# Kernel optimization log

Measured on AMD Instinct MI355X. Metric: run time of the kernel, lower is better.

## Reference

```python
import jax, jax.numpy as jnp
import numpy as np
import math

EPS = 1e-5  # torch LayerNorm default
B, T, H, W, C = 2, 16, 32, 32, 768
NH = 12
HD = C // NH


def layernorm(x, w, b):
    mu = jnp.mean(x, axis=-1, keepdims=True)
    var = jnp.var(x, axis=-1, keepdims=True)
    return (x - mu) * jax.lax.rsqrt(var + EPS) * w + b


def setup_inputs() -> dict:
    key = jax.random.key(0)
    ks = jax.random.split(key, 4)
    s = 1.0 / math.sqrt(C)
    return {
        "x": jax.random.normal(ks[0], (B, T, H, W, C), dtype=jnp.float32),
        "ln1_w": jnp.ones((C,), jnp.float32),
        "ln1_b": jnp.zeros((C,), jnp.float32),
        "Wqkv": jax.random.normal(ks[1], (3 * C, C), jnp.float32) * s,
        "bqkv": jnp.zeros((3 * C,), jnp.float32),
        "ln2_w": jnp.ones((C,), jnp.float32),
        "ln2_b": jnp.zeros((C,), jnp.float32),
        "Wout": jax.random.normal(ks[2], (C, C), jnp.float32) * s,
        "bout": jnp.zeros((C,), jnp.float32),
    }


def reference(x, ln1_w, ln1_b, Wqkv, bqkv, ln2_w, ln2_b, Wout, bout):
    b, t, h, w, c = x.shape
    inp = x
    y = layernorm(x, ln1_w, ln1_b)
    qkv = jnp.einsum('bthwc,fc->bthwf', y, Wqkv) + bqkv          # (B,T,H,W,3C)
    qkv = qkv.reshape(b, t, h, w, NH, 3 * HD)
    q, k, v = jnp.split(qkv, 3, axis=-1)                          # each (B,T,H,W,NH,HD)
    scale = 1.0 / math.sqrt(HD)
    # attention over the time axis, batched over (b,h,w,heads)
    scores = jnp.einsum('bthwnd,bshwnd->bhwnts', q, k) * scale    # (B,H,W,NH,T,T)
    attn = jax.nn.softmax(scores, axis=-1)
    o = jnp.einsum('bhwnts,bshwnd->bthwnd', attn, v)              # (B,T,H,W,NH,HD)
    o = o.reshape(b, t, h, w, c)
    o = layernorm(o, ln2_w, ln2_b)
    o = jnp.einsum('bthwc,fc->bthwf', o, Wout) + bout
    return o + inp
```

## Files before the change

### kernel.cpp

```cpp
#include <hip/hip_runtime.h>

typedef unsigned short u16;
typedef __attribute__((ext_vector_type(8))) short frag8;
typedef __attribute__((ext_vector_type(4))) float f32x4;

static constexpr int C = 768;
static constexpr int F3 = 2304;
static constexpr int MROWS = 32768;
static constexpr float LNEPS = 1e-5f;

__device__ __forceinline__ float bfu2f(u16 u){
  union { unsigned u; float f; } x; x.u = (unsigned)u << 16; return x.f;
}
__device__ __forceinline__ u16 f2bfu(float f){
  union { float f; unsigned u; } x; x.f = f;
  unsigned r = x.u + 0x7fffu + ((x.u >> 16) & 1u);
  return (u16)(r >> 16);
}

__device__ __forceinline__ void gload16(const void* g, void* l){
  __builtin_amdgcn_global_load_lds(
      (const __attribute__((address_space(1))) void*)g,
      (__attribute__((address_space(3))) void*)l, 16, 0, 0);
}

__global__ __launch_bounds__(256) void cvt_bf16(const float* __restrict__ src,
                                                u16* __restrict__ dst, int n){
  int i = blockIdx.x * 256 + threadIdx.x;
  if (i < n) dst[i] = f2bfu(src[i]);
}

__global__ __launch_bounds__(256) void ln1_kernel(const float* __restrict__ x,
    const float* __restrict__ w, const float* __restrict__ b, u16* __restrict__ y){
  const int lane = threadIdx.x & 63, wid = threadIdx.x >> 6;
  const size_t row = (size_t)blockIdx.x * 4 + wid;
  const float4* xr = reinterpret_cast<const float4*>(x + row * C);
  float v[12];
  #pragma unroll
  for (int j = 0; j < 3; j++){
    float4 t = xr[lane + j*64];
    v[j*4+0]=t.x; v[j*4+1]=t.y; v[j*4+2]=t.z; v[j*4+3]=t.w;
  }
  float s = 0.f, ss = 0.f;
  #pragma unroll
  for (int j = 0; j < 12; j++){ s += v[j]; ss += v[j]*v[j]; }
  #pragma unroll
  for (int o = 32; o; o >>= 1){ s += __shfl_xor(s, o, 64); ss += __shfl_xor(ss, o, 64); }
  const float mu = s * (1.f/768.f);
  const float rs = rsqrtf(ss*(1.f/768.f) - mu*mu + LNEPS);
  ushort4* yr = reinterpret_cast<ushort4*>(y + row * C);
  const float4* wv = reinterpret_cast<const float4*>(w);
  const float4* bv = reinterpret_cast<const float4*>(b);
  #pragma unroll
  for (int j = 0; j < 3; j++){
    float4 wj = wv[lane + j*64], bj = bv[lane + j*64];
    ushort4 o4;
    o4.x = f2bfu((v[j*4+0]-mu)*rs*wj.x + bj.x);
    o4.y = f2bfu((v[j*4+1]-mu)*rs*wj.y + bj.y);
    o4.z = f2bfu((v[j*4+2]-mu)*rs*wj.z + bj.z);
    o4.w = f2bfu((v[j*4+3]-mu)*rs*wj.w + bj.w);
    yr[lane + j*64] = o4;
  }
}

template<int MODE>
__global__ __launch_bounds__(256, 2) void gemm_bt(
    const u16* __restrict__ A, const u16* __restrict__ Bw,
    const float* __restrict__ bias, const float* __restrict__ resid,
    void* __restrict__ Cout, int Ndim, int K)
{
  __shared__ __align__(16) char lds[49152];
  const int tid = threadIdx.x;
  const int lane = tid & 63, wn = tid >> 6;
  const int ntn = Ndim >> 8;
  const int cpx = (int)gridDim.x >> 3;
  const int wg = ((int)blockIdx.x & 7) * cpx + ((int)blockIdx.x >> 3);
  const int bm = wg / ntn, bn = wg % ntn;
  const int m0 = bm << 7, n0 = bn << 8;

  const int rp = lane >> 2;
  const int rr = rp ^ ((rp >> 2) & 1);
  const int qq = (lane & 3) ^ (rr & 3);
  const u16* aS = A  + (size_t)(m0 + rr) * K + qq*8;
  const u16* bS = Bw + (size_t)(n0 + rr) * K + qq*8;
  const size_t rgK = 16 * (size_t)K;

  const int fr = lane & 15, kq = lane >> 4;
  const int sig16 = (((fr ^ ((fr >> 2) & 1)) << 2) | (kq ^ (fr & 3))) * 16;

  f32x4 acc[8][4] = {};

  auto stage = [&](int ts){
    char* lb = lds + (ts & 1)*24576;
    const u16* a = aS + ts*32;
    const u16* b = bS + ts*32;
    gload16(a + (size_t)(2*wn    )*rgK, lb + (2*wn    )*1024);
    gload16(a + (size_t)(2*wn + 1)*rgK, lb + (2*wn + 1)*1024);
    #pragma unroll
    for (int i = 0; i < 4; i++)
      gload16(b + (size_t)(4*wn + i)*rgK, lb + 8192 + (4*wn + i)*1024);
  };

  stage(0);

  for (int t = 0; t < 24; ++t){
    int tn = t + 1; if (tn >= 24) tn = 0;
    stage(tn);
    asm volatile("s_waitcnt vmcnt(6)" ::: "memory");
    __builtin_amdgcn_s_barrier();

    const char* base = lds + (t & 1)*24576;
    const char* pb = base + 8192 + (wn*4)*1024 + sig16;
    frag8 af[8], bf[4];
    #pragma unroll
    for (int nf = 0; nf < 4; nf++) bf[nf] = *reinterpret_cast<const frag8*>(pb + nf*1024);
    #pragma unroll
    for (int mf = 0; mf < 8; mf++) af[mf] = *reinterpret_cast<const frag8*>(base + mf*1024 + sig16);
    asm volatile("s_waitcnt lgkmcnt(0)" ::: "memory");
    __builtin_amdgcn_sched_barrier(0);
    __builtin_amdgcn_s_setprio(1);
    #pragma unroll
    for (int mf = 0; mf < 8; mf++)
      #pragma unroll
      for (int nf = 0; nf < 4; nf++)
        acc[mf][nf] = __builtin_amdgcn_mfma_f32_16x16x32_bf16(bf[nf], af[mf], acc[mf][nf], 0, 0, 0);
    __builtin_amdgcn_s_setprio(0);
    __builtin_amdgcn_s_barrier();
  }
  asm volatile("s_waitcnt vmcnt(0)" ::: "memory");

  const int em = fr, en = kq * 4;
  float4 bb[4];
  #pragma unroll
  for (int nf = 0; nf < 4; nf++)
    bb[nf] = *reinterpret_cast<const float4*>(bias + n0 + wn*64 + nf*16 + en);

  #pragma unroll
  for (int mf = 0; mf < 8; mf++){
    const size_t m = (size_t)(m0 + mf*16 + em);
    #pragma unroll
    for (int nf = 0; nf < 4; nf++){
      const int n = n0 + wn*64 + nf*16 + en;
      if (MODE == 0){
        ushort4 o4;
        o4.x = f2bfu(acc[mf][nf][0] + bb[nf].x);
        o4.y = f2bfu(acc[mf][nf][1] + bb[nf].y);
        o4.z = f2bfu(acc[mf][nf][2] + bb[nf].z);
        o4.w = f2bfu(acc[mf][nf][3] + bb[nf].w);
        *reinterpret_cast<ushort4*>((u16*)Cout + m * Ndim + n) = o4;
      } else {
        const float4 rr4 = *reinterpret_cast<const float4*>(resid + m * Ndim + n);
        float4 o4;
        o4.x = acc[mf][nf][0] + bb[nf].x + rr4.x;
        o4.y = acc[mf][nf][1] + bb[nf].y + rr4.y;
        o4.z = acc[mf][nf][2] + bb[nf].z + rr4.z;
        o4.w = acc[mf][nf][3] + bb[nf].w + rr4.w;
        *reinterpret_cast<float4*>((float*)Cout + m * Ndim + n) = o4;
      }
    }
  }
}

__global__ __launch_bounds__(256) void attn_ln2(const u16* __restrict__ qkv,
    const float* __restrict__ w2, const float* __restrict__ b2, u16* __restrict__ y2){
  __shared__ __align__(16) u16 S[16][2312];
  __shared__ float SP[4][16][17];
  const int tid = threadIdx.x;
  const int lane = tid & 63, wid = tid >> 6;
  const int bid = blockIdx.x;
  const int w = bid & 31, h = (bid >> 5) & 31, b = bid >> 10;
  const size_t rbase = (size_t)b*16384 + h*32 + w;

  #pragma unroll
  for (int it = 0; it < 18; it++){
    const int e = tid + it*256;
    const int t = e / 288, c = e % 288;
    const uint4 v = *reinterpret_cast<const uint4*>(qkv + (rbase + (size_t)t*1024)*F3 + c*8);
    *reinterpret_cast<uint4*>(&S[t][c*8]) = v;
  }
  __syncthreads();

  const int g = lane >> 4, sj = lane & 15;
  #pragma unroll
  for (int hh = 0; hh < 3; hh++){
    const int n = wid*3 + hh;
    const int q0 = n*192, k0 = q0 + 64, v0 = q0 + 128;
    float accv[4] = {0.f, 0.f, 0.f, 0.f};
    #pragma unroll
    for (int dc = 0; dc < 8; dc++){
      union { uint4 u; u16 s[8]; } kc;
      kc.u = *reinterpret_cast<const uint4*>(&S[sj][k0 + dc*8]);
      #pragma unroll
      for (int i = 0; i < 4; i++){
        union { uint4 u; u16 s[8]; } qc;
        qc.u = *reinterpret_cast<const uint4*>(&S[g + 4*i][q0 + dc*8]);
        #pragma unroll
        for (int e = 0; e < 8; e++)
          accv[i] += bfu2f(qc.s[e]) * bfu2f(kc.s[e]);
      }
    }
    #pragma unroll
    for (int i = 0; i < 4; i++){
      float sc = accv[i] * 0.125f;
      float mx = sc;
      #pragma unroll
      for (int o = 1; o < 16; o <<= 1) mx = fmaxf(mx, __shfl_xor(mx, o, 16));
      float p = __expf(sc - mx);
      float sm = p;
      #pragma unroll
      for (int o = 1; o < 16; o <<= 1) sm += __shfl_xor(sm, o, 16);
      SP[wid][g + 4*i][sj] = p / sm;
    }
    float ot[16];
    #pragma unroll
    for (int t = 0; t < 16; t++){
      float o = 0.f;
      #pragma unroll
      for (int s = 0; s < 16; s++) o += SP[wid][t][s] * bfu2f(S[s][v0 + lane]);
      ot[t] = o;
    }
    #pragma unroll
    for (int t = 0; t < 16; t++) S[t][v0 + lane] = f2bfu(ot[t]);
  }
  __syncthreads();

  #pragma unroll
  for (int rq = 0; rq < 4; rq++){
    const int t = wid*4 + rq;
    float v[12];
    #pragma unroll
    for (int j = 0; j < 12; j++) v[j] = bfu2f(S[t][j*192 + 128 + lane]);
    float s = 0.f, ss = 0.f;
    #pragma unroll
    for (int j = 0; j < 12; j++){ s += v[j]; ss += v[j]*v[j]; }
    #pragma unroll
    for (int o = 32; o; o >>= 1){ s += __shfl_xor(s, o, 64); ss += __shfl_xor(ss, o, 64); }
    const float mu = s * (1.f/768.f);
    const float rs = rsqrtf(ss*(1.f/768.f) - mu*mu + LNEPS);
    u16* yr = y2 + (rbase + (size_t)t*1024) * C;
    #pragma unroll
    for (int j = 0; j < 12; j++){
      const int c = j*64 + lane;
      yr[c] = f2bfu((v[j]-mu)*rs*w2[c] + b2[c]);
    }
  }
}

extern "C" void kernel_launch(void* const* d_in, const int* in_sizes, int n_in,
                              void* d_out, int out_size, void* d_ws, size_t ws_size,
                              hipStream_t stream){
  const float* x    = (const float*)d_in[0];
  const float* ln1w = (const float*)d_in[1];
  const float* ln1b = (const float*)d_in[2];
  const float* Wqkv = (const float*)d_in[3];
  const float* bqkv = (const float*)d_in[4];
  const float* ln2w = (const float*)d_in[5];
  const float* ln2b = (const float*)d_in[6];
  const float* Wout = (const float*)d_in[7];
  const float* bout = (const float*)d_in[8];
  float* out = (float*)d_out;

  char* ws = (char*)d_ws;
  u16* qkv = (u16*)ws;
  u16* y   = (u16*)(ws + 150994944);
  u16* wq  = (u16*)(ws + 201326592);
  u16* wo  = (u16*)(ws + 204865536);

  cvt_bf16<<<(F3*C + 255)/256, 256, 0, stream>>>(Wqkv, wq, F3*C);
  cvt_bf16<<<(C*C + 255)/256, 256, 0, stream>>>(Wout, wo, C*C);
  ln1_kernel<<<MROWS/4, 256, 0, stream>>>(x, ln1w, ln1b, y);
  gemm_bt<0><<<(MROWS/128)*(F3/256), 256, 0, stream>>>(y, wq, bqkv, nullptr, qkv, F3, C);
  attn_ln2<<<2*32*32, 256, 0, stream>>>(qkv, ln2w, ln2b, y);
  gemm_bt<1><<<(MROWS/128)*(C/256), 256, 0, stream>>>(y, wo, bout, x, out, C, C);
}
```

Before: 337.1 us.

## Use MFMA for time-axis attention with transposed V layout in LDS

Rewrites the attention_ln2 kernel so the QK^T scores and the P·V product run on bf16 MFMA instructions instead of scalar FMA loops. Q and K are packed into a compact LDS tile, and V is stored transposed with zero padding so it can feed MFMA B-fragments. Softmax probabilities stay in registers and are shuffled into fragment layout, and the launch bounds request two blocks per CU. This lowers LDS footprint and ALU work, but adds an extra rounding of probabilities to bf16 and a strided scalar transpose store into LDS.

```diff
diff --git a/kernel.cpp b/kernel.cpp
--- a/kernel.cpp
+++ b/kernel.cpp
@@ -161,10 +161,10 @@
   }
 }
 
-__global__ __launch_bounds__(256) void attn_ln2(const u16* __restrict__ qkv,
+__global__ __launch_bounds__(256, 2) void attn_ln2(const u16* __restrict__ qkv,
     const float* __restrict__ w2, const float* __restrict__ b2, u16* __restrict__ y2){
-  __shared__ __align__(16) u16 S[16][2312];
-  __shared__ float SP[4][16][17];
+  __shared__ __align__(16) u16 S[16][1544];
+  __shared__ __align__(16) u16 Vt[15376];
   const int tid = threadIdx.x;
   const int lane = tid & 63, wid = tid >> 6;
   const int bid = blockIdx.x;
@@ -172,55 +172,92 @@
   const size_t rbase = (size_t)b*16384 + h*32 + w;
 
   #pragma unroll
-  for (int it = 0; it < 18; it++){
+  for (int i = 0; i < 4; i++){
+    const int idx = tid + i*256;
+    if (idx < 772){
+      const int off = (idx < 768) ? ((idx >> 6)*1280 + (idx & 63)*20 + 16)
+                                  : (15360 + (idx - 768)*4);
+      uint2 z; z.x = 0u; z.y = 0u;
+      *reinterpret_cast<uint2*>(&Vt[off]) = z;
+    }
+  }
+
+  #pragma unroll
+  for (int it = 0; it < 12; it++){
     const int e = tid + it*256;
-    const int t = e / 288, c = e % 288;
-    const uint4 v = *reinterpret_cast<const uint4*>(qkv + (rbase + (size_t)t*1024)*F3 + c*8);
-    *reinterpret_cast<uint4*>(&S[t][c*8]) = v;
+    const int t = e / 192, c = e % 192;
+    const int n = c >> 4, p = c & 15;
+    const uint4 v = *reinterpret_cast<const uint4*>(qkv + (rbase + (size_t)t*1024)*F3 + (n*24 + p)*8);
+    *reinterpret_cast<uint4*>(&S[t][n*128 + p*8]) = v;
+  }
+  #pragma unroll
+  for (int it = 0; it < 6; it++){
+    const int e = tid + it*256;
+    const int t = e / 96, c = e % 96;
+    const int n = c >> 3, j = c & 7;
+    union { uint4 u; u16 s[8]; } vv;
+    vv.u = *reinterpret_cast<const uint4*>(qkv + (rbase + (size_t)t*1024)*F3 + (n*24 + 16 + j)*8);
+    #pragma unroll
+    for (int x = 0; x < 8; x++)
+      Vt[n*1280 + (j*8 + x)*20 + t] = vv.s[x];
   }
   __syncthreads();
 
-  const int g = lane >> 4, sj = lane & 15;
+  const int q = lane >> 4, tcol = lane & 15;
+  unsigned pf[3][4];
+
   #pragma unroll
   for (int hh = 0; hh < 3; hh++){
     const int n = wid*3 + hh;
-    const int q0 = n*192, k0 = q0 + 64, v0 = q0 + 128;
-    float accv[4] = {0.f, 0.f, 0.f, 0.f};
-    #pragma unroll
-    for (int dc = 0; dc < 8; dc++){
-      union { uint4 u; u16 s[8]; } kc;
-      kc.u = *reinterpret_cast<const uint4*>(&S[sj][k0 + dc*8]);
-      #pragma unroll
-      for (int i = 0; i < 4; i++){
-        union { uint4 u; u16 s[8]; } qc;
-        qc.u = *reinterpret_cast<const uint4*>(&S[g + 4*i][q0 + dc*8]);
-        #pragma unroll
-        for (int e = 0; e < 8; e++)
-          accv[i] += bfu2f(qc.s[e]) * bfu2f(kc.s[e]);
-      }
+    const int qc = n*128, kc = n*128 + 64;
+    frag8 qf0 = *reinterpret_cast<const frag8*>(&S[tcol][qc + q*8]);
+    frag8 qf1 = *reinterpret_cast<const frag8*>(&S[tcol][qc + 32 + q*8]);
+    frag8 kf0 = *reinterpret_cast<const frag8*>(&S[tcol][kc + q*8]);
+    frag8 kf1 = *reinterpret_cast<const frag8*>(&S[tcol][kc + 32 + q*8]);
+    f32x4 sa = {};
+    sa = __builtin_amdgcn_mfma_f32_16x16x32_bf16(kf0, qf0, sa, 0, 0, 0);
+    sa = __builtin_amdgcn_mfma_f32_16x16x32_bf16(kf1, qf1, sa, 0, 0, 0);
+    const float sc0 = sa[0]*0.125f, sc1 = sa[1]*0.125f;
+    const float sc2 = sa[2]*0.125f, sc3 = sa[3]*0.125f;
+    float mx = fmaxf(fmaxf(sc0, sc1), fmaxf(sc2, sc3));
+    mx = fmaxf(mx, __shfl_xor(mx, 16, 64));
+    mx = fmaxf(mx, __shfl_xor(mx, 32, 64));
+    float p0 = __expf(sc0-mx), p1 = __expf(sc1-mx), p2 = __expf(sc2-mx), p3 = __expf(sc3-mx);
+    float sm = p0+p1+p2+p3;
+    sm += __shfl_xor(sm, 16, 64);
+    sm += __shfl_xor(sm, 32, 64);
+    const float inv = 1.f / sm;
+    const unsigned b0 = (unsigned)f2bfu(p0*inv) | ((unsigned)f2bfu(p1*inv) << 16);
+    const unsigned b1 = (unsigned)f2bfu(p2*inv) | ((unsigned)f2bfu(p3*inv) << 16);
+    const unsigned t0 = __shfl((unsigned)b0, (lane+16)&63, 64);
+    const unsigned t1 = __shfl((unsigned)b1, (lane+16)&63, 64);
+    const unsigned t2 = __shfl((unsigned)b0, (lane+32)&63, 64);
+    const unsigned t3 = __shfl((unsigned)b1, (lane+32)&63, 64);
+    pf[hh][0] = (q==0) ? b0 : ((q==1) ? t0 : 0u);
+    pf[hh][1] = (q==0) ? b1 : ((q==1) ? t1 : 0u);
+    pf[hh][2] = (q==0) ? t0 : ((q==1) ? t2 : 0u);
+    pf[hh][3] = (q==0) ? t1 : ((q==1) ? t3 : 0u);
+  }
+  __syncthreads();
+
+  #pragma unroll
+  for (int hh = 0; hh < 3; hh++){
+    const int n = wid*3 + hh;
+    union { frag8 f; unsigned u[4]; } pu;
+    pu.u[0] = pf[hh][0]; pu.u[1] = pf[hh][1]; pu.u[2] = pf[hh][2]; pu.u[3] = pf[hh][3];
+    #pragma unroll
+    for (int dcv = 0; dcv < 4; dcv++){
+      union { frag8 f; uint2 v2[2]; } vf;
+      const int vi = n*1280 + (dcv*16 + tcol)*20 + q*8;
+      vf.v2[0] = *reinterpret_cast<const uint2*>(&Vt[vi]);
+      vf.v2[1] = *reinterpret_cast<const uint2*>(&Vt[vi + 4]);
+      f32x4 oa = {};
+      oa = __builtin_amdgcn_mfma_f32_16x16x32_bf16(vf.f, pu.f, oa, 0, 0, 0);
+      uint2 ow;
+      ow.x = (unsigned)f2bfu(oa[0]) | ((unsigned)f2bfu(oa[1]) << 16);
+      ow.y = (unsigned)f2bfu(oa[2]) | ((unsigned)f2bfu(oa[3]) << 16);
+      *reinterpret_cast<uint2*>(&S[tcol][n*64 + dcv*16 + q*4]) = ow;
     }
-    #pragma unroll
-    for (int i = 0; i < 4; i++){
-      float sc = accv[i] * 0.125f;
-      float mx = sc;
-      #pragma unroll
-      for (int o = 1; o < 16; o <<= 1) mx = fmaxf(mx, __shfl_xor(mx, o, 16));
-      float p = __expf(sc - mx);
-      float sm = p;
-      #pragma unroll
-      for (int o = 1; o < 16; o <<= 1) sm += __shfl_xor(sm, o, 16);
-      SP[wid][g + 4*i][sj] = p / sm;
-    }
-    float ot[16];
-    #pragma unroll
-    for (int t = 0; t < 16; t++){
-      float o = 0.f;
-      #pragma unroll
-      for (int s = 0; s < 16; s++) o += SP[wid][t][s] * bfu2f(S[s][v0 + lane]);
-      ot[t] = o;
-    }
-    #pragma unroll
-    for (int t = 0; t < 16; t++) S[t][v0 + lane] = f2bfu(ot[t]);
   }
   __syncthreads();
 
@@ -229,7 +266,7 @@
     const int t = wid*4 + rq;
     float v[12];
     #pragma unroll
-    for (int j = 0; j < 12; j++) v[j] = bfu2f(S[t][j*192 + 128 + lane]);
+    for (int j = 0; j < 12; j++) v[j] = bfu2f(S[t][j*64 + lane]);
     float s = 0.f, ss = 0.f;
     #pragma unroll
     for (int j = 0; j < 12; j++){ s += v[j]; ss += v[j]*v[j]; }
```

Measured after the change: 316.5 us. 1.07x faster.
